# Optimization experiments

Measured on AMD Instinct MI355X. Metric: run time of the kernel, lower is better.

The kernel has to match this reference:

```python
import jax, jax.numpy as jnp
import numpy as np

D_HID = 1024
N_HEADS = 16
D_HEAD = D_HID // N_HEADS


def setup_inputs() -> dict:
    key = jax.random.key(0)
    k_x, k_w, k_b = jax.random.split(key, 3)
    x = jax.random.normal(k_x, (8, 4096, D_HID), dtype=jnp.float32)
    # qkv linear params (torch Linear: y = x @ W.T + b; we store W already transposed)
    W_qkv = jax.random.normal(k_w, (D_HID, 3 * D_HID), dtype=jnp.float32) / np.sqrt(D_HID)
    b_qkv = jax.random.normal(k_b, (3 * D_HID,), dtype=jnp.float32) * 0.01
    return {"x": x, "W_qkv": W_qkv, "b_qkv": b_qkv}


def reference(x, W_qkv, b_qkv):
    B, N, _ = x.shape
    qkv = x @ W_qkv + b_qkv  # [B, N, 3*d_hid]
    q, k, v = jnp.split(qkv, 3, axis=-1)

    def heads(t):  # [B, N, d_hid] -> [B, H, N, d_head]
        return t.reshape(B, N, N_HEADS, D_HEAD).transpose(0, 2, 1, 3)

    q, k, v = heads(q), heads(k), heads(v)
    # channel attention: contract over sequence N -> [B, H, d_head, d_head]
    attn = jnp.einsum("bhnd,bhne->bhde", q, k) / np.sqrt(D_HEAD)
    attn = jax.nn.softmax(attn, axis=-1)  # softmax over channel dim
    # outputs = V @ attn : [B, H, N, d_head]
    out = jnp.einsum("bhnd,bhde->bhne", v, attn)
    out = out.transpose(0, 2, 1, 3).reshape(B, N, N_HEADS * D_HEAD)
    return out
```

## Files before the change

### kernel.cpp

```cpp
#include <hip/hip_runtime.h>
#include <hip/hip_bf16.h>


typedef __attribute__((ext_vector_type(4))) float  f32x4;
typedef __attribute__((ext_vector_type(8))) short  bf16x8;
typedef __attribute__((ext_vector_type(8))) unsigned short u16x8;

typedef __attribute__((address_space(1))) const unsigned int GBUF;
typedef __attribute__((address_space(3))) unsigned int       LBUF;

#define DEVI __device__ __forceinline__

static constexpr int BATCH = 8;
static constexpr int NSEQ  = 4096;
static constexpr int DHID  = 1024;
static constexpr int NHEAD = 16;
static constexpr int DH    = 64;
static constexpr int MROWS = BATCH * NSEQ;
static constexpr int N3    = 3 * DHID;

DEVI unsigned short f2bf(float f) {
    unsigned int u = __float_as_uint(f);
    u = (u + 0x7fffu + ((u >> 16) & 1u)) >> 16;
    return (unsigned short)u;
}

__global__ void k_cvt_x(const float* __restrict__ x, unsigned short* __restrict__ xb, int n8) {
    int i = blockIdx.x * 256 + threadIdx.x;
    int stride = gridDim.x * 256;
    for (; i < n8; i += stride) {
        f32x4 a = *(const f32x4*)(x + (size_t)i * 8);
        f32x4 b = *(const f32x4*)(x + (size_t)i * 8 + 4);
        u16x8 r;
#pragma unroll
        for (int j = 0; j < 4; j++) { r[j] = f2bf(a[j]); r[4 + j] = f2bf(b[j]); }
        *(u16x8*)(xb + (size_t)i * 8) = r;
    }
}

__global__ void k_wt(const float* __restrict__ W, unsigned short* __restrict__ Wt) {
    __shared__ float s[32][33];
    int c0 = blockIdx.x * 32;
    int k0 = blockIdx.y * 32;
    int tx = threadIdx.x & 31, ty = threadIdx.x >> 5;
#pragma unroll
    for (int i = 0; i < 4; i++)
        s[ty + 8 * i][tx] = W[(size_t)(k0 + ty + 8 * i) * N3 + c0 + tx];
    __syncthreads();
#pragma unroll
    for (int i = 0; i < 4; i++)
        Wt[(size_t)(c0 + ty + 8 * i) * DHID + k0 + tx] = f2bf(s[tx][ty + 8 * i]);
}

__global__ __launch_bounds__(512, 2) void k_gemm1(
        const unsigned short* __restrict__ xb, const unsigned short* __restrict__ Wt,
        const float* __restrict__ bias,
        unsigned short* __restrict__ Q, unsigned short* __restrict__ Kw,
        unsigned short* __restrict__ V) {
    __shared__ __align__(16) unsigned short As[2][16384];
    __shared__ __align__(16) unsigned short Bs[2][16384];

    int nwg = gridDim.x;
    int cpx = nwg >> 3;
    int id  = blockIdx.x;
    int swz = (id & 7) * cpx + (id >> 3);
    int mt = swz / 12, nt = swz % 12;
    int m0 = mt * 256, n0 = nt * 256;

    int t = threadIdx.x, l = t & 63, w = t >> 6;
    int wr = w >> 2, wc = w & 3;
    int lr = l & 15;

    const unsigned short* aSrc = xb + (size_t)m0 * DHID;
    const unsigned short* bSrc = Wt + (size_t)n0 * DHID;

    int scol = ((t & 7) * 8) ^ (((t >> 3) & 7) << 3);
    int c0 = ((l >> 4) * 8) ^ ((l & 7) << 3);
    int aRow = wr * 128 + lr;
    int bRow = wc * 64 + lr;

#define STAGE_A(bi, kt, h) do { \
        const unsigned short* _s = aSrc + (size_t)((h) * 128 + (t >> 3)) * DHID + (kt) * 64 + scol; \
        unsigned short* _d = &As[bi][(h) * 8192 + t * 8]; \
        __builtin_amdgcn_global_load_lds((GBUF*)_s, (LBUF*)_d, 16, 0, 0); \
        __builtin_amdgcn_global_load_lds((GBUF*)(_s + 64 * DHID), (LBUF*)(_d + 4096), 16, 0, 0); \
    } while (0)
#define STAGE_B(bi, kt, h) do { \
        const unsigned short* _s = bSrc + (size_t)((h) * 128 + (t >> 3)) * DHID + (kt) * 64 + scol; \
        unsigned short* _d = &Bs[bi][(h) * 8192 + t * 8]; \
        __builtin_amdgcn_global_load_lds((GBUF*)_s, (LBUF*)_d, 16, 0, 0); \
        __builtin_amdgcn_global_load_lds((GBUF*)(_s + 64 * DHID), (LBUF*)(_d + 4096), 16, 0, 0); \
    } while (0)
#define LDA(bi, dst, mh) \
    _Pragma("unroll") for (int m2 = 0; m2 < 4; m2++) { \
        const unsigned short* _row = &As[bi][(aRow + (mh) * 64 + m2 * 16) * 64]; \
        dst[m2][0] = *(const bf16x8*)(_row + c0); \
        dst[m2][1] = *(const bf16x8*)(_row + (c0 ^ 32)); \
    }
#define LDB(bi, dst, nh) \
    _Pragma("unroll") for (int n2 = 0; n2 < 2; n2++) { \
        const unsigned short* _row = &Bs[bi][(bRow + (nh) * 32 + n2 * 16) * 64]; \
        dst[n2][0] = *(const bf16x8*)(_row + c0); \
        dst[n2][1] = *(const bf16x8*)(_row + (c0 ^ 32)); \
    }
#define MM(mh, nh, A_, B_) \
    _Pragma("unroll") for (int m2 = 0; m2 < 4; m2++) \
    _Pragma("unroll") for (int n2 = 0; n2 < 2; n2++) { \
        acc[(mh)*4+m2][(nh)*2+n2] = __builtin_amdgcn_mfma_f32_16x16x32_bf16(A_[m2][0], B_[n2][0], acc[(mh)*4+m2][(nh)*2+n2], 0, 0, 0); \
        acc[(mh)*4+m2][(nh)*2+n2] = __builtin_amdgcn_mfma_f32_16x16x32_bf16(A_[m2][1], B_[n2][1], acc[(mh)*4+m2][(nh)*2+n2], 0, 0, 0); \
    }
#define BAR __builtin_amdgcn_s_barrier()
#define LGKM0 do { asm volatile("s_waitcnt lgkmcnt(0)" ::: "memory"); \
                   __builtin_amdgcn_sched_barrier(0); } while (0)
#define VM4 asm volatile("s_waitcnt vmcnt(4)" ::: "memory")
#define PRIO1 __builtin_amdgcn_s_setprio(1)
#define PRIO0 __builtin_amdgcn_s_setprio(0)

    f32x4 acc[8][4] = {};
    bf16x8 fA0[4][2], fA1[4][2], fB0[2][2], fB1[2][2];

    STAGE_A(0, 0, 0); STAGE_A(0, 0, 1);
    STAGE_B(0, 0, 0); STAGE_B(0, 0, 1);
    STAGE_A(1, 1, 0); STAGE_A(1, 1, 1);
    VM4;
    BAR;

#pragma unroll 1
    for (int i = 0; i < 8; ++i) {
        int kc1 = 2 * i + 1;
        int kn0 = (2 * i + 2) & 15, kn1 = (2 * i + 3) & 15;
        LDA(0, fA0, 0); LDB(0, fB0, 0); STAGE_B(1, kc1, 0);
        BAR; LGKM0; PRIO1; MM(0, 0, fA0, fB0); PRIO0; BAR;

        LDA(0, fA1, 1); STAGE_B(1, kc1, 1);
        BAR; LGKM0; PRIO1; MM(1, 0, fA1, fB0); PRIO0; BAR;

        LDB(0, fB1, 1); STAGE_A(0, kn0, 0);
        BAR; LGKM0; PRIO1; MM(1, 1, fA1, fB1); PRIO0; BAR;

        STAGE_A(0, kn0, 1);
        BAR; PRIO1; MM(0, 1, fA0, fB1); PRIO0;
        VM4;
        BAR;
        LDA(1, fA0, 0); LDB(1, fB0, 0); STAGE_B(0, kn0, 0);
        BAR; LGKM0; PRIO1; MM(0, 0, fA0, fB0); PRIO0; BAR;

        LDA(1, fA1, 1); STAGE_B(0, kn0, 1);
        BAR; LGKM0; PRIO1; MM(1, 0, fA1, fB0); PRIO0; BAR;

        LDB(1, fB1, 1); STAGE_A(1, kn1, 0);
        BAR; LGKM0; PRIO1; MM(1, 1, fA1, fB1); PRIO0; BAR;

        STAGE_A(1, kn1, 1);
        BAR; PRIO1; MM(0, 1, fA0, fB1); PRIO0;
        VM4;
        BAR;
    }

    int hg   = nt * 4 + wc;
    int part = hg >> 4;
    int h    = hg & 15;
    unsigned short* dst = (part == 0) ? Q : ((part == 1) ? Kw : V);
    int b   = m0 >> 12;
    int nnb = m0 & 4095;
    unsigned short* dstp = dst + ((size_t)(b * 16 + h) * NSEQ) * DH;

#pragma unroll
    for (int n = 0; n < 4; n++) {
        int e    = n * 16 + lr;
        float bv = bias[n0 + wc * 64 + n * 16 + lr];
#pragma unroll
        for (int m = 0; m < 8; m++) {
            int r0 = nnb + wr * 128 + m * 16 + (l >> 4) * 4;
#pragma unroll
            for (int j = 0; j < 4; j++)
                dstp[(size_t)(r0 + j) * DH + e] = f2bf(acc[m][n][j] + bv);
        }
    }
#undef STAGE_A
#undef STAGE_B
#undef LDA
#undef LDB
#undef MM
#undef BAR
#undef LGKM0
#undef VM4
#undef PRIO1
#undef PRIO0
}

__global__ __launch_bounds__(256, 2) void k_qk(
        const unsigned short* __restrict__ Q, const unsigned short* __restrict__ K,
        float* __restrict__ part) {
    __shared__ unsigned short Qt[64 * 40];
    __shared__ unsigned short Kt[64 * 40];

    int bid = blockIdx.x;
    int bh = bid >> 2, ch = bid & 3;
    const unsigned short* Qb = Q + ((size_t)bh * NSEQ + ch * 1024) * DH;
    const unsigned short* Kb = K + ((size_t)bh * NSEQ + ch * 1024) * DH;

    int t = threadIdx.x, l = t & 63, w = t >> 6;
    int wr = w >> 1, wc = w & 1;
    int nn = t & 31;
    int dg = t >> 5;

    f32x4 acc[2][2] = {};

    for (int ns = 0; ns < 32; ns++) {
        const size_t ro = (size_t)(ns * 32 + nn) * DH + dg * 8;
        bf16x8 qv = *(const bf16x8*)(Qb + ro);
        bf16x8 kv = *(const bf16x8*)(Kb + ro);
        __syncthreads();
#pragma unroll
        for (int j = 0; j < 8; j++) {
            Qt[(dg * 8 + j) * 40 + nn] = qv[j];
            Kt[(dg * 8 + j) * 40 + nn] = kv[j];
        }
        __syncthreads();
        bf16x8 a[2], b[2];
#pragma unroll
        for (int m = 0; m < 2; m++)
            a[m] = *(const bf16x8*)(Qt + (wr * 32 + m * 16 + (l & 15)) * 40 + (l >> 4) * 8);
#pragma unroll
        for (int n = 0; n < 2; n++)
            b[n] = *(const bf16x8*)(Kt + (wc * 32 + n * 16 + (l & 15)) * 40 + (l >> 4) * 8);
#pragma unroll
        for (int m = 0; m < 2; m++)
#pragma unroll
            for (int n = 0; n < 2; n++)
                acc[m][n] = __builtin_amdgcn_mfma_f32_16x16x32_bf16(a[m], b[n], acc[m][n], 0, 0, 0);
    }

    float* P = part + ((size_t)ch * 128 + bh) * 4096;
#pragma unroll
    for (int m = 0; m < 2; m++)
#pragma unroll
        for (int n = 0; n < 2; n++)
#pragma unroll
            for (int j = 0; j < 4; j++) {
                int d = wr * 32 + m * 16 + (l >> 4) * 4 + j;
                int e = wc * 32 + n * 16 + (l & 15);
                P[d * 64 + e] = acc[m][n][j];
            }
}

__global__ void k_softmax(const float* __restrict__ part, unsigned short* __restrict__ attn_t) {
    int bh = blockIdx.x;
    int d  = threadIdx.x;
    const float* p = part + (size_t)bh * 4096 + d * 64;
    const size_t cs = (size_t)128 * 4096;
    float s[64];
#pragma unroll
    for (int e = 0; e < 64; e++)
        s[e] = (p[e] + p[cs + e] + p[2 * cs + e] + p[3 * cs + e]) * 0.125f;
    float mx = s[0];
#pragma unroll
    for (int e = 1; e < 64; e++) mx = fmaxf(mx, s[e]);
    float sum = 0.f;
#pragma unroll
    for (int e = 0; e < 64; e++) { s[e] = __expf(s[e] - mx); sum += s[e]; }
    float inv = 1.f / sum;
    unsigned short* a = attn_t + (size_t)bh * 4096;
#pragma unroll
    for (int e = 0; e < 64; e++)
        a[e * 64 + d] = f2bf(s[e] * inv);
}

__global__ __launch_bounds__(256, 2) void k_out(
        const unsigned short* __restrict__ V, const unsigned short* __restrict__ attn_t,
        float* __restrict__ out) {
    int bid = blockIdx.x;
    int bh = bid >> 4, ntile = bid & 15;
    int b = bh >> 4, h = bh & 15;
    int t = threadIdx.x, l = t & 63, w = t >> 6;
    int r0 = ntile * 256 + w * 64;

    const unsigned short* Vb = V + (size_t)bh * NSEQ * DH;
    const unsigned short* Ab = attn_t + (size_t)bh * 4096;

    bf16x8 bf[4][2];
#pragma unroll
    for (int n = 0; n < 4; n++)
#pragma unroll
        for (int ks = 0; ks < 2; ks++)
            bf[n][ks] = *(const bf16x8*)(Ab + (n * 16 + (l & 15)) * 64 + ks * 32 + (l >> 4) * 8);

    f32x4 acc[4][4] = {};
#pragma unroll
    for (int m = 0; m < 4; m++) {
        const unsigned short* vr = Vb + (size_t)(r0 + m * 16 + (l & 15)) * DH + (l >> 4) * 8;
        bf16x8 av0 = *(const bf16x8*)(vr);
        bf16x8 av1 = *(const bf16x8*)(vr + 32);
#pragma unroll
        for (int n = 0; n < 4; n++) {
            acc[m][n] = __builtin_amdgcn_mfma_f32_16x16x32_bf16(av0, bf[n][0], acc[m][n], 0, 0, 0);
            acc[m][n] = __builtin_amdgcn_mfma_f32_16x16x32_bf16(av1, bf[n][1], acc[m][n], 0, 0, 0);
        }
    }

    float* ob = out + (size_t)b * NSEQ * DHID + (size_t)h * DH;
#pragma unroll
    for (int m = 0; m < 4; m++)
#pragma unroll
        for (int n = 0; n < 4; n++)
#pragma unroll
            for (int j = 0; j < 4; j++) {
                int nn = r0 + m * 16 + (l >> 4) * 4 + j;
                int e  = n * 16 + (l & 15);
                ob[(size_t)nn * DHID + e] = acc[m][n][j];
            }
}

extern "C" void kernel_launch(void* const* d_in, const int* in_sizes, int n_in,
                              void* d_out, int out_size, void* d_ws, size_t ws_size,
                              hipStream_t stream) {
    const float* x    = (const float*)d_in[0];
    const float* W    = (const float*)d_in[1];
    const float* bias = (const float*)d_in[2];
    float* out = (float*)d_out;

    char* wsp = (char*)d_ws;
    unsigned short* xb   = (unsigned short*)(wsp);
    unsigned short* Wt   = (unsigned short*)(wsp + 67108864);
    unsigned short* Qw   = (unsigned short*)(wsp + 73400320);
    unsigned short* Kww  = (unsigned short*)(wsp + 140509184);
    unsigned short* Vw   = (unsigned short*)(wsp + 207618048);
    float*          part = (float*)(wsp + 274726912);
    unsigned short* attn = (unsigned short*)(wsp + 283115520);

    k_cvt_x<<<2048, 256, 0, stream>>>(x, xb, MROWS * DHID / 8);
    k_wt<<<dim3(N3 / 32, DHID / 32), 256, 0, stream>>>(W, Wt);
    k_gemm1<<<(MROWS / 256) * (N3 / 256), 512, 0, stream>>>(xb, Wt, bias, Qw, Kww, Vw);
    k_qk<<<128 * 4, 256, 0, stream>>>(Qw, Kww, part);
    k_softmax<<<128, 64, 0, stream>>>(part, attn);
    k_out<<<128 * 16, 256, 0, stream>>>(Vw, attn, out);
}
```

Baseline: 611.9 us.

## Stage QKV GEMM epilogue through swizzled LDS and prefetch next tile in k_qk

The QKV projection epilogue now writes bias-added bf16 results into the reused A/B shared-memory buffers with an XOR swizzle, then stores them to global memory as contiguous 16-byte vectors instead of scattered 2-byte stores. The goal is to replace many uncoalesced narrow global writes with fully coalesced wide writes. It adds a vmcnt(0) wait and a barrier before the epilogue. Separately, k_qk software-prefetches the next Q/K tile into registers so global load latency overlaps with the MFMA work on the current tile, at the cost of extra registers and one wasted wraparound load.

```diff
diff --git a/kernel.cpp b/kernel.cpp
--- a/kernel.cpp
+++ b/kernel.cpp
@@ -113,6 +113,7 @@
 #define LGKM0 do { asm volatile("s_waitcnt lgkmcnt(0)" ::: "memory"); \
                    __builtin_amdgcn_sched_barrier(0); } while (0)
 #define VM4 asm volatile("s_waitcnt vmcnt(4)" ::: "memory")
+#define VM0 asm volatile("s_waitcnt vmcnt(0)" ::: "memory")
 #define PRIO1 __builtin_amdgcn_s_setprio(1)
 #define PRIO0 __builtin_amdgcn_s_setprio(0)
 
@@ -156,6 +157,9 @@
         VM4;
         BAR;
     }
+
+    VM0;
+    BAR;
 
     int hg   = nt * 4 + wc;
     int part = hg >> 4;
@@ -165,17 +169,30 @@
     int nnb = m0 & 4095;
     unsigned short* dstp = dst + ((size_t)(b * 16 + h) * NSEQ) * DH;
 
-#pragma unroll
-    for (int n = 0; n < 4; n++) {
-        int e    = n * 16 + lr;
-        float bv = bias[n0 + wc * 64 + n * 16 + lr];
-#pragma unroll
-        for (int m = 0; m < 8; m++) {
-            int r0 = nnb + wr * 128 + m * 16 + (l >> 4) * 4;
-#pragma unroll
-            for (int j = 0; j < 4; j++)
-                dstp[(size_t)(r0 + j) * DH + e] = f2bf(acc[m][n][j] + bv);
-        }
+    unsigned short* eb = (w < 4) ? (&As[0][0] + w * 8192) : (&Bs[0][0] + (w - 4) * 8192);
+
+    float bv[4];
+#pragma unroll
+    for (int n = 0; n < 4; n++) bv[n] = bias[n0 + wc * 64 + n * 16 + lr];
+
+#pragma unroll
+    for (int n = 0; n < 4; n++)
+#pragma unroll
+        for (int m = 0; m < 8; m++)
+#pragma unroll
+            for (int j = 0; j < 4; j++) {
+                int lm = m * 16 + (l >> 4) * 4 + j;
+                eb[lm * 64 + ((n * 16 + lr) ^ (((lm >> 2) & 3) << 4))] =
+                    f2bf(acc[m][n][j] + bv[n]);
+            }
+
+    const size_t base2 = (size_t)(nnb + wr * 128) * DH;
+#pragma unroll
+    for (int rr = 0; rr < 16; rr++) {
+        int u = rr * 64 + l;
+        int row = u >> 3, unit = u & 7;
+        bf16x8 v = *(const bf16x8*)&eb[row * 64 + ((unit * 8) ^ (((row >> 2) & 3) << 4))];
+        *(bf16x8*)(dstp + base2 + (size_t)u * 8) = v;
     }
 #undef STAGE_A
 #undef STAGE_B
@@ -185,6 +202,7 @@
 #undef BAR
 #undef LGKM0
 #undef VM4
+#undef VM0
 #undef PRIO1
 #undef PRIO0
 }
@@ -207,10 +225,14 @@
 
     f32x4 acc[2][2] = {};
 
+    size_t ro0 = (size_t)nn * DH + dg * 8;
+    bf16x8 qv = *(const bf16x8*)(Qb + ro0);
+    bf16x8 kv = *(const bf16x8*)(Kb + ro0);
+
     for (int ns = 0; ns < 32; ns++) {
-        const size_t ro = (size_t)(ns * 32 + nn) * DH + dg * 8;
-        bf16x8 qv = *(const bf16x8*)(Qb + ro);
-        bf16x8 kv = *(const bf16x8*)(Kb + ro);
+        const size_t rn = (size_t)((((ns + 1) & 31) * 32) + nn) * DH + dg * 8;
+        bf16x8 qn = *(const bf16x8*)(Qb + rn);
+        bf16x8 kn = *(const bf16x8*)(Kb + rn);
         __syncthreads();
 #pragma unroll
         for (int j = 0; j < 8; j++) {
@@ -230,6 +252,7 @@
 #pragma unroll
             for (int n = 0; n < 2; n++)
                 acc[m][n] = __builtin_amdgcn_mfma_f32_16x16x32_bf16(a[m], b[n], acc[m][n], 0, 0, 0);
+        qv = qn; kv = kn;
     }
 
     float* P = part + ((size_t)ch * 128 + bh) * 4096;
```

Result: faster. 547.4 us (-10.5%).
